# Optimization experiments

Hardware: AMD Instinct MI355X
Metric: run time of the kernel (lower is better)

The kernel has to match this reference:

```python
import jax, jax.numpy as jnp
import numpy as np
import math

B, S, HID = 2, 2048, 1536
H, HD = 12, 128           # num_heads, head_dim
LAT = HID // 8            # latent_dim = 192
ROT = HD // 2             # 64, rotary applied to this half-size subspace


def _make_rotary(seq_len, dim=ROT, base=10000.0):
    # LlamaRotaryEmbedding: inv_freq over dim/2 freqs, emb = cat(sin, cos) -> [1,1,S,dim]
    inv_freq = 1.0 / (base ** (np.arange(0, dim, 2, dtype=np.float32) / dim))
    pos = np.arange(seq_len, dtype=np.float32)
    sincos = np.einsum('i,j->ij', pos, inv_freq)  # [S, dim/2]
    emb = np.concatenate([np.sin(sincos), np.cos(sincos)], axis=-1)  # [S, dim]
    return jnp.asarray(emb)[None, None, :, :]


def setup_inputs() -> dict:
    key = jax.random.key(0)
    ks = jax.random.split(key, 10)
    sd = 0.02
    return {
        'hidden_states': jax.random.normal(ks[0], (B, S, HID), jnp.float32),
        'rotary_emb': _make_rotary(S),
        'W_kv_d':  jax.random.normal(ks[1], (HID, LAT), jnp.float32) * sd,
        'W_q_d':   jax.random.normal(ks[2], (HID, LAT), jnp.float32) * sd,
        'W_k_u':   jax.random.normal(ks[3], (LAT, H * ROT), jnp.float32) * sd,
        'W_q_u':   jax.random.normal(ks[4], (LAT, H * ROT), jnp.float32) * sd,
        'W_v_u':   jax.random.normal(ks[5], (LAT, H * HD), jnp.float32) * sd,
        'W_rope_k': jax.random.normal(ks[6], (HID, HID // 2), jnp.float32) * sd,
        'W_rope_q': jax.random.normal(ks[7], (LAT, HID // 2), jnp.float32) * sd,
        'W_o':     jax.random.normal(ks[8], (HID, HID), jnp.float32) * sd,
    }


def _apply_rope(x, emb):
    # x: [B,S,H,ROT]; emb: [1,1,S,ROT] (cat of sin,cos, each ROT/2)
    half = ROT // 2
    x1, x2 = x[..., :half], x[..., half:]
    sin = emb[..., :half].transpose(0, 2, 1, 3)  # -> [1,S,1,half] to broadcast over heads
    cos = emb[..., half:].transpose(0, 2, 1, 3)
    return jnp.concatenate([x1 * cos - x2 * sin, x1 * sin + x2 * cos], axis=-1)


def reference(hidden_states, rotary_emb, W_kv_d, W_q_d, W_k_u, W_q_u, W_v_u,
              W_rope_k, W_rope_q, W_o):
    b, s, _ = hidden_states.shape
    kv_d = hidden_states @ W_kv_d                       # [B,S,LAT]
    q_d = hidden_states @ W_q_d                         # [B,S,LAT]
    k_c = (kv_d @ W_k_u).reshape(b, s, H, ROT)          # content half of K
    q_c = (q_d @ W_q_u).reshape(b, s, H, ROT)
    v = (kv_d @ W_v_u).reshape(b, s, H, HD)
    k_r = (hidden_states @ W_rope_k).reshape(b, s, H, ROT)
    q_r = (q_d @ W_rope_q).reshape(b, s, H, ROT)
    k_r = _apply_rope(k_r, rotary_emb)
    q_r = _apply_rope(q_r, rotary_emb)
    k = jnp.concatenate([k_c, k_r], axis=-1)            # [B,S,H,HD]
    q = jnp.concatenate([q_c, q_r], axis=-1)

    scores = jnp.einsum('bqhd,bkhd->bhqk', q, k) / math.sqrt(HD)
    causal = jnp.tril(jnp.ones((s, s), dtype=bool))
    scores = jnp.where(causal[None, None], scores, jnp.float32(-1e9))
    probs = jax.nn.softmax(scores, axis=-1)
    attn = jnp.einsum('bhqk,bkhd->bqhd', probs, v).reshape(b, s, HID)
    return attn @ W_o
```

## Files before the change

### kernel.cpp

```cpp
#include <hip/hip_runtime.h>
#include <hip/hip_bf16.h>

#define B_ 2
#define S_ 2048
#define HID_ 1536
#define H_ 12
#define HD_ 128
#define LAT_ 192
#define ROT_ 64
#define M_ (B_*S_)

typedef __hip_bfloat16 bf16;

using short8  = __attribute__((ext_vector_type(8))) short;
using short4v = __attribute__((ext_vector_type(4))) short;
using float4v = __attribute__((ext_vector_type(4))) float;

__device__ __forceinline__ unsigned short f2bf(float f) {
  __hip_bfloat16 h = __float2bfloat16(f);
  unsigned short u; __builtin_memcpy(&u, &h, 2); return u;
}

#define GLDS16(gp, lp) __builtin_amdgcn_global_load_lds( \
    (__attribute__((address_space(1))) void*)(size_t)(gp), \
    (__attribute__((address_space(3))) void*)(lp), 16, 0, 0)

__global__ __launch_bounds__(256)
void fillf_k(float* __restrict__ out, float v, int n)
{
  int i = blockIdx.x*256 + threadIdx.x;
  if (i < n) out[i] = v;
}

__global__ __launch_bounds__(256)
void packT4_k(const float* __restrict__ s0, const float* __restrict__ s1,
              const float* __restrict__ s2, const float* __restrict__ s3,
              bf16* __restrict__ d0, bf16* __restrict__ d1,
              bf16* __restrict__ d2, bf16* __restrict__ d3,
              int Kn, int N0, int N1, int N2, int N3)
{
  const float* W; bf16* Wt; int Nn;
  switch (blockIdx.z) {
    case 0:  W = s0; Wt = d0; Nn = N0; break;
    case 1:  W = s1; Wt = d1; Nn = N1; break;
    case 2:  W = s2; Wt = d2; Nn = N2; break;
    default: W = s3; Wt = d3; Nn = N3; break;
  }
  const int kb = blockIdx.x*32, nb = blockIdx.y*32;
  if (nb >= Nn) return;
  __shared__ float t[32][33];
  const int tx = threadIdx.x & 31, ty = threadIdx.x >> 5;
  #pragma unroll
  for (int i = 0; i < 4; i++)
    t[ty+8*i][tx] = W[(size_t)(kb+ty+8*i)*Nn + nb + tx];
  __syncthreads();
  #pragma unroll
  for (int i = 0; i < 4; i++)
    Wt[(size_t)(nb + ty + 8*i)*Kn + kb + tx] = __float2bfloat16(t[tx][ty+8*i]);
}

template<int CMODE, int BM, int AF32>
__global__ __launch_bounds__(256)
void gemm_mfma(const void* __restrict__ Av, const bf16* __restrict__ Bt,
               void* __restrict__ Cv, void* __restrict__ Cv2,
               const float* __restrict__ emb, int Kn, int lda, int ldb, int ldc)
{
  constexpr int MI  = BM/32;
  constexpr int ITA = BM/32;
  __shared__ bf16 As[(size_t)BM*64];
  __shared__ bf16 Bs[128*64];

  const int tid  = threadIdx.x;
  const int lane = tid & 63;
  const int w    = tid >> 6;
  const int col  = lane & 15, quad = lane >> 4;
  const int wr   = w >> 1, wc = w & 1;
  const size_t m0 = (size_t)blockIdx.y * BM;
  const size_t n0 = (size_t)blockIdx.x * 128;

  const bf16* bg[4];
  #pragma unroll
  for (int it = 0; it < 4; it++) {
    int c = tid + it*256, row = c >> 3, seg = c & 7;
    bg[it] = Bt + (n0 + row)*ldb + (size_t)((seg ^ (row & 7))*8);
  }
  const bf16* ag[ITA];
  const float* asrc = nullptr;
  int arow = 0;
  if constexpr (AF32) {
    arow = tid >> 2;
    const int aseg = tid & 3;
    asrc = (const float*)Av + (m0 + arow)*lda + aseg*16;
  } else {
    #pragma unroll
    for (int it = 0; it < ITA; it++) {
      int c = tid + it*256, row = c >> 3, seg = c & 7;
      ag[it] = (const bf16*)Av + (m0 + row)*lda + (size_t)((seg ^ (row & 7))*8);
    }
  }

  float4v acc[MI][4];
  #pragma unroll
  for (int i=0;i<MI;i++)
    #pragma unroll
    for (int j=0;j<4;j++) acc[i][j] = (float4v){0.f,0.f,0.f,0.f};

  for (int k0 = 0; k0 < Kn; k0 += 64) {
    #pragma unroll
    for (int it = 0; it < 4; it++)
      GLDS16(bg[it] + k0, Bs + (size_t)(tid + it*256)*8);
    if constexpr (AF32) {
      const int aseg = tid & 3;
      float4 f0 = *(const float4*)(asrc + k0);
      float4 f1 = *(const float4*)(asrc + k0 + 4);
      float4 f2 = *(const float4*)(asrc + k0 + 8);
      float4 f3 = *(const float4*)(asrc + k0 + 12);
      short8 h0, h1;
      h0[0]=(short)f2bf(f0.x); h0[1]=(short)f2bf(f0.y);
      h0[2]=(short)f2bf(f0.z); h0[3]=(short)f2bf(f0.w);
      h0[4]=(short)f2bf(f1.x); h0[5]=(short)f2bf(f1.y);
      h0[6]=(short)f2bf(f1.z); h0[7]=(short)f2bf(f1.w);
      h1[0]=(short)f2bf(f2.x); h1[1]=(short)f2bf(f2.y);
      h1[2]=(short)f2bf(f2.z); h1[3]=(short)f2bf(f2.w);
      h1[4]=(short)f2bf(f3.x); h1[5]=(short)f2bf(f3.y);
      h1[6]=(short)f2bf(f3.z); h1[7]=(short)f2bf(f3.w);
      const int sl0 = (aseg*2) ^ (arow & 7), sl1 = (aseg*2+1) ^ (arow & 7);
      *(short8*)&As[arow*64 + sl0*8] = h0;
      *(short8*)&As[arow*64 + sl1*8] = h1;
    } else {
      #pragma unroll
      for (int it = 0; it < ITA; it++)
        GLDS16(ag[it] + k0, As + (size_t)(tid + it*256)*8);
    }
    __syncthreads();

    short8 af[MI][2], bfr[4][2];
    #pragma unroll
    for (int i=0;i<MI;i++) {
      const int ar = wr*(BM/2) + i*16 + col;
      #pragma unroll
      for (int k2=0;k2<2;k2++)
        af[i][k2] = *(const short8*)&As[ar*64 + ((k2*4+quad)^(ar&7))*8];
    }
    #pragma unroll
    for (int j=0;j<4;j++) {
      const int br = wc*64 + j*16 + col;
      #pragma unroll
      for (int k2=0;k2<2;k2++)
        bfr[j][k2] = *(const short8*)&Bs[br*64 + ((k2*4+quad)^(br&7))*8];
    }

    #pragma unroll
    for (int k2=0;k2<2;k2++)
      #pragma unroll
      for (int i=0;i<MI;i++)
        #pragma unroll
        for (int j=0;j<4;j++)
          acc[i][j] = __builtin_amdgcn_mfma_f32_16x16x32_bf16(af[i][k2], bfr[j][k2], acc[i][j], 0,0,0);
    __syncthreads();
  }

  if constexpr (CMODE == 0) {
    #pragma unroll
    for (int i=0;i<MI;i++) {
      const size_t row0 = m0 + wr*(BM/2) + i*16 + quad*4;
      #pragma unroll
      for (int j=0;j<4;j++) {
        const int c = (int)n0 + wc*64 + j*16 + col;
        #pragma unroll
        for (int r=0;r<4;r++)
          ((float*)Cv)[(row0+r)*ldc + c] = acc[i][j][r];
      }
    }
    return;
  }

  constexpr int RBASE = (CMODE == 5) ? 384 : 768;
  if ((int)n0 < RBASE) {
    #pragma unroll
    for (int i=0;i<MI;i++) {
      const size_t row0 = m0 + wr*(BM/2) + i*16 + quad*4;
      #pragma unroll
      for (int j=0;j<4;j++) {
        const int c = (int)n0 + wc*64 + j*16 + col;
        #pragma unroll
        for (int r=0;r<4;r++) {
          const float v = acc[i][j][r];
          if constexpr (CMODE == 5)
            ((bf16*)Cv)[(row0+r)*384 + c] = __float2bfloat16(v);
          else
            ((bf16*)Cv)[(row0+r)*HID_ + (c>>6)*HD_ + (c&63)] = __float2bfloat16(v);
        }
      }
    }
  } else if constexpr (CMODE == 3) {
    #pragma unroll
    for (int i=0;i<MI;i++) {
      const size_t row0 = m0 + wr*(BM/2) + i*16 + quad*4;
      const int bb = (int)(row0 >> 11), s = (int)(row0 & (S_-1));
      #pragma unroll
      for (int j=0;j<4;j++) {
        const int cv = (int)n0 - 768 + wc*64 + j*16 + col;
        const int hh = cv >> 7, d = cv & 127;
        short4v st;
        #pragma unroll
        for (int r=0;r<4;r++) st[r] = (short)f2bf(acc[i][j][r]);
        *(short4v*)((unsigned short*)Cv2 +
            ((size_t)(bb*H_+hh)*HD_ + d)*S_ + s) = st;
      }
    }
  } else {
    const int hh = (((int)n0 - RBASE) >> 6) + wc;
    #pragma unroll
    for (int i=0;i<MI;i++) {
      const size_t row0 = m0 + wr*(BM/2) + i*16 + quad*4;
      #pragma unroll
      for (int j=0;j<2;j++) {
        const int idim = j*16 + col;
        #pragma unroll
        for (int r=0;r<4;r++) {
          const size_t row = row0 + r;
          const int s = (int)(row & (S_-1));
          const float sn = emb[(size_t)s*ROT_ + idim];
          const float cs = emb[(size_t)s*ROT_ + 32 + idim];
          const float x1 = acc[i][j][r], x2 = acc[i][j+2][r];
          bf16* dst = (bf16*)Cv2 + (row*H_ + hh)*HD_ + 64 + idim;
          dst[0]  = __float2bfloat16(x1*cs - x2*sn);
          dst[32] = __float2bfloat16(x1*sn + x2*cs);
        }
      }
    }
  }
}

#define KSTR 136
#define VSTR 72
#define PSTR 72

__global__ __launch_bounds__(256)
void attn_mfma(const bf16* __restrict__ Qf, const bf16* __restrict__ Kf,
               const bf16* __restrict__ Vtg, bf16* __restrict__ at)
{
  const int qt = (S_/64 - 1) - (int)(blockIdx.x / (B_*H_));
  const int bh = blockIdx.x % (B_*H_);
  const int h  = bh % H_, b = bh / H_;
  const int tid  = threadIdx.x;
  const int w    = tid >> 6;
  const int lane = tid & 63;
  const int col  = lane & 15;
  const int quad = lane >> 4;

  __shared__ unsigned short Ks[64*KSTR];
  __shared__ unsigned short Vt[128*VSTR];
  __shared__ unsigned short Ps[4][16*PSTR];

  const int q0  = qt * 64;
  const int q0w = q0 + w*16;

  const unsigned short* Kb = (const unsigned short*)Kf +
      ((size_t)b*S_*H_ + h)*HD_;
  const unsigned short* Vb = (const unsigned short*)Vtg +
      (size_t)(b*H_ + h)*HD_*S_;

  const unsigned short* kgp[4]; unsigned short* kdst[4];
  const unsigned short* vgp[4]; unsigned short* vdst[4];
  #pragma unroll
  for (int it = 0; it < 4; it++) {
    int c = tid + it*256;
    int key = c >> 4, doff = (c & 15)*8;
    kgp[it]  = Kb + (size_t)key*HID_ + doff;
    kdst[it] = &Ks[key*KSTR + doff];
    int d = c >> 3, kg = (c & 7)*8;
    vgp[it]  = Vb + (size_t)d*S_ + kg;
    vdst[it] = &Vt[d*VSTR + kg];
  }

  short8 qf[4];
  {
    const unsigned short* qrow = (const unsigned short*)Qf +
        ((size_t)((size_t)b*S_ + q0w + col)*H_ + h)*HD_;
    #pragma unroll
    for (int kk = 0; kk < 4; kk++)
      qf[kk] = *(const short8*)(qrow + kk*32 + quad*8);
  }

  float4v O[8];
  #pragma unroll
  for (int t=0;t<8;t++) O[t] = (float4v){0.f,0.f,0.f,0.f};
  float m_ln = -1e30f, l_ln = 0.f;

  const float scale2 = 0.08838834764831845f * 1.4426950408889634f;

  short8 kr[4], vr[4];
  #pragma unroll
  for (int it = 0; it < 4; it++) {
    kr[it] = *(const short8*)kgp[it];
    vr[it] = *(const short8*)vgp[it];
  }

  for (int kb = 0; kb <= qt; kb++) {
    const int k0 = kb * 64;
    const bool diag = (kb == qt);

    #pragma unroll
    for (int it = 0; it < 4; it++) *(short8*)kdst[it] = kr[it];
    #pragma unroll
    for (int it = 0; it < 4; it++) *(short8*)vdst[it] = vr[it];
    __syncthreads();

    if (!diag) {
      const size_t kn = (size_t)(k0 + 64);
      #pragma unroll
      for (int it = 0; it < 4; it++) {
        kr[it] = *(const short8*)(kgp[it] + kn*HID_);
        vr[it] = *(const short8*)(vgp[it] + kn);
      }
    }

    float4v Sf[4];
    #pragma unroll
    for (int tc=0;tc<4;tc++) Sf[tc] = (float4v){0.f,0.f,0.f,0.f};
    __builtin_amdgcn_s_setprio(1);
    if (!diag) {
      #pragma unroll
      for (int tc = 0; tc < 4; tc++)
        #pragma unroll
        for (int kk = 0; kk < 4; kk++) {
          short8 kfrag = *(const short8*)&Ks[(16*tc+col)*KSTR + 32*kk + quad*8];
          Sf[tc] = __builtin_amdgcn_mfma_f32_16x16x32_bf16(kfrag, qf[kk], Sf[tc], 0,0,0);
        }
    } else {
      #pragma unroll
      for (int tc = 0; tc < 4; tc++) {
        if (tc <= w) {
          #pragma unroll
          for (int kk = 0; kk < 4; kk++) {
            short8 kfrag = *(const short8*)&Ks[(16*tc+col)*KSTR + 32*kk + quad*8];
            Sf[tc] = __builtin_amdgcn_mfma_f32_16x16x32_bf16(kfrag, qf[kk], Sf[tc], 0,0,0);
          }
        }
      }
    }
    __builtin_amdgcn_s_setprio(0);

    float sv[4][4];
    float pmax = -3.0e38f;
    if (!diag) {
      #pragma unroll
      for (int tc = 0; tc < 4; tc++)
        #pragma unroll
        for (int r = 0; r < 4; r++) {
          float s = Sf[tc][r] * scale2;
          sv[tc][r] = s;
          pmax = fmaxf(pmax, s);
        }
    } else {
      const int qrel = w*16 + col;
      #pragma unroll
      for (int tc = 0; tc < 4; tc++)
        #pragma unroll
        for (int r = 0; r < 4; r++) {
          float s = Sf[tc][r] * scale2;
          if (tc*16 + quad*4 + r > qrel) s = -3.0e38f;
          sv[tc][r] = s;
          pmax = fmaxf(pmax, s);
        }
    }
    pmax = fmaxf(pmax, __shfl_xor(pmax, 16));
    pmax = fmaxf(pmax, __shfl_xor(pmax, 32));

    if (__all(pmax <= m_ln + 11.0f)) {
      float lt = 0.f;
      #pragma unroll
      for (int tc = 0; tc < 4; tc++)
        #pragma unroll
        for (int r = 0; r < 4; r++) {
          sv[tc][r] = exp2f(sv[tc][r] - m_ln);
          lt += sv[tc][r];
        }
      lt += __shfl_xor(lt, 16);
      lt += __shfl_xor(lt, 32);
      l_ln += lt;
    } else {
      const float mnew = fmaxf(m_ln, pmax);
      float lt = 0.f;
      #pragma unroll
      for (int tc = 0; tc < 4; tc++)
        #pragma unroll
        for (int r = 0; r < 4; r++) {
          sv[tc][r] = exp2f(sv[tc][r] - mnew);
          lt += sv[tc][r];
        }
      lt += __shfl_xor(lt, 16);
      lt += __shfl_xor(lt, 32);
      const float al = exp2f(m_ln - mnew);
      l_ln = l_ln * al + lt;
      m_ln = mnew;
      float alr[4];
      #pragma unroll
      for (int r = 0; r < 4; r++) alr[r] = __shfl(al, quad*4 + r);
      #pragma unroll
      for (int t = 0; t < 8; t++)
        #pragma unroll
        for (int r = 0; r < 4; r++) O[t][r] *= alr[r];
    }

    #pragma unroll
    for (int tc = 0; tc < 4; tc++) {
      short4v pw;
      pw[0] = (short)f2bf(sv[tc][0]); pw[1] = (short)f2bf(sv[tc][1]);
      pw[2] = (short)f2bf(sv[tc][2]); pw[3] = (short)f2bf(sv[tc][3]);
      *(short4v*)&Ps[w][col*PSTR + tc*16 + quad*4] = pw;
    }

    __builtin_amdgcn_s_setprio(1);
    if (!diag) {
      #pragma unroll
      for (int ks = 0; ks < 2; ks++) {
        short8 pf = *(const short8*)&Ps[w][col*PSTR + 32*ks + quad*8];
        #pragma unroll
        for (int t = 0; t < 8; t++) {
          short8 vf = *(const short8*)&Vt[(16*t + col)*VSTR + 32*ks + quad*8];
          O[t] = __builtin_amdgcn_mfma_f32_16x16x32_bf16(pf, vf, O[t], 0,0,0);
        }
      }
    } else {
      #pragma unroll
      for (int ks = 0; ks < 2; ks++) {
        if (ks == 0 || w >= 2) {
          short8 pf = *(const short8*)&Ps[w][col*PSTR + 32*ks + quad*8];
          #pragma unroll
          for (int t = 0; t < 8; t++) {
            short8 vf = *(const short8*)&Vt[(16*t + col)*VSTR + 32*ks + quad*8];
            O[t] = __builtin_amdgcn_mfma_f32_16x16x32_bf16(pf, vf, O[t], 0,0,0);
          }
        }
      }
    }
    __builtin_amdgcn_s_setprio(0);
    __syncthreads();
  }

  float lr[4];
  #pragma unroll
  for (int r = 0; r < 4; r++) lr[r] = __shfl(l_ln, quad*4 + r);
  #pragma unroll
  for (int r = 0; r < 4; r++) {
    const float linv = 1.f / lr[r];
    const size_t mq = (size_t)b*S_ + q0w + quad*4 + r;
    bf16* dst = at + mq*HID_ + h*HD_ + col;
    #pragma unroll
    for (int t = 0; t < 8; t++)
      dst[16*t] = __float2bfloat16(O[t][r] * linv);
  }
}

extern "C" void kernel_launch(void* const* d_in, const int* in_sizes, int n_in,
                              void* d_out, int out_size, void* d_ws, size_t ws_size,
                              hipStream_t stream)
{
  float* out = (float*)d_out;

  static const int sz_dict[10] = {6291456,131072,294912,294912,147456,
                                  147456,294912,1179648,147456,2359296};
  int bad = -1;
  if (n_in < 10) bad = 15;
  else {
    for (int i = 0; i < 10; i++)
      if (in_sizes[i] != sz_dict[i]) { bad = i; break; }
  }
  if (bad >= 0) {
    float v = 1.0e6f * (float)(1 + bad);
    if (bad < 10) v += (float)(in_sizes[bad] % 1000000);
    fillf_k<<<(out_size + 255)/256, 256, 0, stream>>>(out, v, out_size);
    return;
  }

  const float* hidden = (const float*)d_in[0];
  const float* emb    = (const float*)d_in[1];
  const float* Wkvd   = (const float*)d_in[2];
  const float* Wqd    = (const float*)d_in[3];
  const float* Wku    = (const float*)d_in[4];
  const float* Wqu    = (const float*)d_in[5];
  const float* Wvu    = (const float*)d_in[6];
  const float* Wrk    = (const float*)d_in[7];
  const float* Wrq    = (const float*)d_in[8];
  const float* Wo     = (const float*)d_in[9];

  char* wp = (char*)d_ws;
  size_t used = 0;
  auto alloc = [&](size_t bytes) -> void* {
    void* p = wp + used;
    used += (bytes + 255) & ~(size_t)255;
    return p;
  };
  bf16*  dout  = (bf16*)alloc((size_t)M_*384*2);
  bf16*  Kf    = (bf16*)alloc((size_t)M_*HID_*2);
  bf16*  Qf    = (bf16*)alloc((size_t)M_*HID_*2);
  bf16*  Vtg   = (bf16*)alloc((size_t)B_*H_*HD_*S_*2);
  bf16*  at    = (bf16*)alloc((size_t)M_*HID_*2);
  bf16*  WdkrT = (bf16*)alloc((size_t)1152*HID_*2);
  bf16*  WkvuT = (bf16*)alloc((size_t)2304*LAT_*2);
  bf16*  WqurT = (bf16*)alloc((size_t)1536*LAT_*2);
  bf16*  WoT   = (bf16*)alloc((size_t)HID_*HID_*2);

  if (used > ws_size) {
    fillf_k<<<(out_size + 255)/256, 256, 0, stream>>>(out, 5.0e7f, out_size);
    return;
  }

  packT4_k<<<dim3(48,48,4), 256, 0, stream>>>(
      Wkvd, Wqd, Wrk, Wo,
      WdkrT, WdkrT + (size_t)192*HID_, WdkrT + (size_t)384*HID_, WoT,
      HID_, LAT_, LAT_, H_*ROT_, HID_);
  packT4_k<<<dim3(6,48,4), 256, 0, stream>>>(
      Wku, Wvu, Wqu, Wrq,
      WkvuT, WkvuT + (size_t)768*LAT_, WqurT, WqurT + (size_t)768*LAT_,
      LAT_, H_*ROT_, HID_, H_*ROT_, H_*ROT_);

  gemm_mfma<5,64,1><<<dim3(9, M_/64),  256, 0, stream>>>(hidden, WdkrT, dout, Kf, emb, HID_, HID_, HID_, 0);
  gemm_mfma<3,64,0><<<dim3(18, M_/64), 256, 0, stream>>>(dout,     WkvuT, Kf, Vtg, emb, LAT_, 384, LAT_, 0);
  gemm_mfma<4,64,0><<<dim3(12, M_/64), 256, 0, stream>>>(dout+192, WqurT, Qf, Qf,  emb, LAT_, 384, LAT_, 0);

  attn_mfma<<<B_*H_*(S_/64), 256, 0, stream>>>(Qf, Kf, Vtg, at);

  gemm_mfma<0,128,0><<<dim3(HID_/128, M_/128), 256, 0, stream>>>(at, WoT, out, nullptr, emb, HID_, HID_, HID_, HID_);
}
```

Measured before the change: 266.5 us.

## Pre-convert hidden to bf16, merge up-projection GEMMs, persistent attention scheduler

Hidden states are converted to bf16 once inside the weight-packing kernel, so the first GEMM loads A through direct global-to-LDS copies and uses 128-row tiles. The two up-projection GEMMs (KV and Q) are merged into a single launch that picks its operands by column range. Attention becomes a persistent kernel of 512 blocks that take tiles from an atomic counter, longest causal tiles first, to balance load. The cost is an extra bf16 copy of the hidden states in memory, a memset, and one atomic per tile.

```diff
diff --git a/kernel.cpp b/kernel.cpp
--- a/kernel.cpp
+++ b/kernel.cpp
@@ -9,6 +9,7 @@
 #define LAT_ 192
 #define ROT_ 64
 #define M_ (B_*S_)
+#define NTILE_ (B_*H_*(S_/64))
 
 typedef __hip_bfloat16 bf16;
 
@@ -33,12 +34,26 @@
 }
 
 __global__ __launch_bounds__(256)
-void packT4_k(const float* __restrict__ s0, const float* __restrict__ s1,
+void packT5_k(const float* __restrict__ s0, const float* __restrict__ s1,
               const float* __restrict__ s2, const float* __restrict__ s3,
               bf16* __restrict__ d0, bf16* __restrict__ d1,
               bf16* __restrict__ d2, bf16* __restrict__ d3,
-              int Kn, int N0, int N1, int N2, int N3)
+              int Kn, int N0, int N1, int N2, int N3,
+              const float* __restrict__ hsrc, bf16* __restrict__ hdst)
 {
+  if (blockIdx.z == 4) {
+    const int nblk = gridDim.x * gridDim.y;
+    const int flatb = blockIdx.y * gridDim.x + blockIdx.x;
+    const float4* in4 = (const float4*)hsrc;
+    for (int i = flatb*256 + threadIdx.x; i < M_*HID_/4; i += nblk*256) {
+      float4 v = in4[i];
+      short4v o;
+      o[0] = (short)f2bf(v.x); o[1] = (short)f2bf(v.y);
+      o[2] = (short)f2bf(v.z); o[3] = (short)f2bf(v.w);
+      *(short4v*)&hdst[i*4] = o;
+    }
+    return;
+  }
   const float* W; bf16* Wt; int Nn;
   switch (blockIdx.z) {
     case 0:  W = s0; Wt = d0; Nn = N0; break;
@@ -59,10 +74,12 @@
     Wt[(size_t)(nb + ty + 8*i)*Kn + kb + tx] = __float2bfloat16(t[tx][ty+8*i]);
 }
 
-template<int CMODE, int BM, int AF32>
+template<int CMODE, int BM>
 __global__ __launch_bounds__(256)
-void gemm_mfma(const void* __restrict__ Av, const bf16* __restrict__ Bt,
+void gemm_mfma(const bf16* __restrict__ Av, const bf16* __restrict__ Btp,
+               const bf16* __restrict__ Av2, const bf16* __restrict__ Bt2,
                void* __restrict__ Cv, void* __restrict__ Cv2,
+               void* __restrict__ Cv3,
                const float* __restrict__ emb, int Kn, int lda, int ldb, int ldc)
 {
   constexpr int MI  = BM/32;
@@ -78,25 +95,24 @@
   const size_t m0 = (size_t)blockIdx.y * BM;
   const size_t n0 = (size_t)blockIdx.x * 128;
 
+  const bf16* Abase = Av;
+  const bf16* Bt    = Btp;
+  size_t nrow0 = n0;
+  if constexpr (CMODE == 6) {
+    if ((int)n0 >= 2304) { Abase = Av2; Bt = Bt2; nrow0 = n0 - 2304; }
+  }
+
   const bf16* bg[4];
   #pragma unroll
   for (int it = 0; it < 4; it++) {
     int c = tid + it*256, row = c >> 3, seg = c & 7;
-    bg[it] = Bt + (n0 + row)*ldb + (size_t)((seg ^ (row & 7))*8);
+    bg[it] = Bt + (nrow0 + row)*ldb + (size_t)((seg ^ (row & 7))*8);
   }
   const bf16* ag[ITA];
-  const float* asrc = nullptr;
-  int arow = 0;
-  if constexpr (AF32) {
-    arow = tid >> 2;
-    const int aseg = tid & 3;
-    asrc = (const float*)Av + (m0 + arow)*lda + aseg*16;
-  } else {
-    #pragma unroll
-    for (int it = 0; it < ITA; it++) {
-      int c = tid + it*256, row = c >> 3, seg = c & 7;
-      ag[it] = (const bf16*)Av + (m0 + row)*lda + (size_t)((seg ^ (row & 7))*8);
-    }
+  #pragma unroll
+  for (int it = 0; it < ITA; it++) {
+    int c = tid + it*256, row = c >> 3, seg = c & 7;
+    ag[it] = Abase + (m0 + row)*lda + (size_t)((seg ^ (row & 7))*8);
   }
 
   float4v acc[MI][4];
@@ -109,29 +125,9 @@
     #pragma unroll
     for (int it = 0; it < 4; it++)
       GLDS16(bg[it] + k0, Bs + (size_t)(tid + it*256)*8);
-    if constexpr (AF32) {
-      const int aseg = tid & 3;
-      float4 f0 = *(const float4*)(asrc + k0);
-      float4 f1 = *(const float4*)(asrc + k0 + 4);
-      float4 f2 = *(const float4*)(asrc + k0 + 8);
-      float4 f3 = *(const float4*)(asrc + k0 + 12);
-      short8 h0, h1;
-      h0[0]=(short)f2bf(f0.x); h0[1]=(short)f2bf(f0.y);
-      h0[2]=(short)f2bf(f0.z); h0[3]=(short)f2bf(f0.w);
-      h0[4]=(short)f2bf(f1.x); h0[5]=(short)f2bf(f1.y);
-      h0[6]=(short)f2bf(f1.z); h0[7]=(short)f2bf(f1.w);
-      h1[0]=(short)f2bf(f2.x); h1[1]=(short)f2bf(f2.y);
-      h1[2]=(short)f2bf(f2.z); h1[3]=(short)f2bf(f2.w);
-      h1[4]=(short)f2bf(f3.x); h1[5]=(short)f2bf(f3.y);
-      h1[6]=(short)f2bf(f3.z); h1[7]=(short)f2bf(f3.w);
-      const int sl0 = (aseg*2) ^ (arow & 7), sl1 = (aseg*2+1) ^ (arow & 7);
-      *(short8*)&As[arow*64 + sl0*8] = h0;
-      *(short8*)&As[arow*64 + sl1*8] = h1;
-    } else {
-      #pragma unroll
-      for (int it = 0; it < ITA; it++)
-        GLDS16(ag[it] + k0, As + (size_t)(tid + it*256)*8);
-    }
+    #pragma unroll
+    for (int it = 0; it < ITA; it++)
+      GLDS16(ag[it] + k0, As + (size_t)(tid + it*256)*8);
     __syncthreads();
 
     short8 af[MI][2], bfr[4][2];
@@ -175,8 +171,45 @@
     return;
   }
 
-  constexpr int RBASE = (CMODE == 5) ? 384 : 768;
-  if ((int)n0 < RBASE) {
+  if constexpr (CMODE == 5) {
+    if ((int)n0 < 384) {
+      #pragma unroll
+      for (int i=0;i<MI;i++) {
+        const size_t row0 = m0 + wr*(BM/2) + i*16 + quad*4;
+        #pragma unroll
+        for (int j=0;j<4;j++) {
+          const int c = (int)n0 + wc*64 + j*16 + col;
+          #pragma unroll
+          for (int r=0;r<4;r++)
+            ((bf16*)Cv)[(row0+r)*384 + c] = __float2bfloat16(acc[i][j][r]);
+        }
+      }
+    } else {
+      const int hh = (((int)n0 - 384) >> 6) + wc;
+      #pragma unroll
+      for (int i=0;i<MI;i++) {
+        const size_t row0 = m0 + wr*(BM/2) + i*16 + quad*4;
+        #pragma unroll
+        for (int j=0;j<2;j++) {
+          const int idim = j*16 + col;
+          #pragma unroll
+          for (int r=0;r<4;r++) {
+            const size_t row = row0 + r;
+            const int s = (int)(row & (S_-1));
+            const float sn = emb[(size_t)s*ROT_ + idim];
+            const float cs = emb[(size_t)s*ROT_ + 32 + idim];
+            const float x1 = acc[i][j][r], x2 = acc[i][j+2][r];
+            bf16* dst = (bf16*)Cv2 + (row*H_ + hh)*HD_ + 64 + idim;
+            dst[0]  = __float2bfloat16(x1*cs - x2*sn);
+            dst[32] = __float2bfloat16(x1*sn + x2*cs);
+          }
+        }
+      }
+    }
+    return;
+  }
+
+  if ((int)n0 < 768) {
     #pragma unroll
     for (int i=0;i<MI;i++) {
       const size_t row0 = m0 + wr*(BM/2) + i*16 + quad*4;
@@ -184,16 +217,11 @@
       for (int j=0;j<4;j++) {
         const int c = (int)n0 + wc*64 + j*16 + col;
         #pragma unroll
-        for (int r=0;r<4;r++) {
-          const float v = acc[i][j][r];
-          if constexpr (CMODE == 5)
-            ((bf16*)Cv)[(row0+r)*384 + c] = __float2bfloat16(v);
-          else
-            ((bf16*)Cv)[(row0+r)*HID_ + (c>>6)*HD_ + (c&63)] = __float2bfloat16(v);
-        }
-      }
-    }
-  } else if constexpr (CMODE == 3) {
+        for (int r=0;r<4;r++)
+          ((bf16*)Cv)[(row0+r)*HID_ + (c>>6)*HD_ + (c&63)] = __float2bfloat16(acc[i][j][r]);
+      }
+    }
+  } else if ((int)n0 < 2304) {
     #pragma unroll
     for (int i=0;i<MI;i++) {
       const size_t row0 = m0 + wr*(BM/2) + i*16 + quad*4;
@@ -209,8 +237,20 @@
             ((size_t)(bb*H_+hh)*HD_ + d)*S_ + s) = st;
       }
     }
+  } else if ((int)n0 < 3072) {
+    #pragma unroll
+    for (int i=0;i<MI;i++) {
+      const size_t row0 = m0 + wr*(BM/2) + i*16 + quad*4;
+      #pragma unroll
+      for (int j=0;j<4;j++) {
+        const int c = (int)n0 - 2304 + wc*64 + j*16 + col;
+        #pragma unroll
+        for (int r=0;r<4;r++)
+          ((bf16*)Cv3)[(row0+r)*HID_ + (c>>6)*HD_ + (c&63)] = __float2bfloat16(acc[i][j][r]);
+      }
+    }
   } else {
-    const int hh = (((int)n0 - RBASE) >> 6) + wc;
+    const int hh = (((int)n0 - 3072) >> 6) + wc;
     #pragma unroll
     for (int i=0;i<MI;i++) {
       const size_t row0 = m0 + wr*(BM/2) + i*16 + quad*4;
@@ -224,7 +264,7 @@
           const float sn = emb[(size_t)s*ROT_ + idim];
           const float cs = emb[(size_t)s*ROT_ + 32 + idim];
           const float x1 = acc[i][j][r], x2 = acc[i][j+2][r];
-          bf16* dst = (bf16*)Cv2 + (row*H_ + hh)*HD_ + 64 + idim;
+          bf16* dst = (bf16*)Cv3 + (row*H_ + hh)*HD_ + 64 + idim;
           dst[0]  = __float2bfloat16(x1*cs - x2*sn);
           dst[32] = __float2bfloat16(x1*sn + x2*cs);
         }
@@ -239,11 +279,9 @@
 
 __global__ __launch_bounds__(256)
 void attn_mfma(const bf16* __restrict__ Qf, const bf16* __restrict__ Kf,
-               const bf16* __restrict__ Vtg, bf16* __restrict__ at)
+               const bf16* __restrict__ Vtg, bf16* __restrict__ at,
+               int* __restrict__ qcnt)
 {
-  const int qt = (S_/64 - 1) - (int)(blockIdx.x / (B_*H_));
-  const int bh = blockIdx.x % (B_*H_);
-  const int h  = bh % H_, b = bh / H_;
   const int tid  = threadIdx.x;
   const int w    = tid >> 6;
   const int lane = tid & 63;
@@ -253,181 +291,180 @@
   __shared__ unsigned short Ks[64*KSTR];
   __shared__ unsigned short Vt[128*VSTR];
   __shared__ unsigned short Ps[4][16*PSTR];
-
-  const int q0  = qt * 64;
-  const int q0w = q0 + w*16;
-
-  const unsigned short* Kb = (const unsigned short*)Kf +
-      ((size_t)b*S_*H_ + h)*HD_;
-  const unsigned short* Vb = (const unsigned short*)Vtg +
-      (size_t)(b*H_ + h)*HD_*S_;
-
-  const unsigned short* kgp[4]; unsigned short* kdst[4];
-  const unsigned short* vgp[4]; unsigned short* vdst[4];
-  #pragma unroll
-  for (int it = 0; it < 4; it++) {
-    int c = tid + it*256;
-    int key = c >> 4, doff = (c & 15)*8;
-    kgp[it]  = Kb + (size_t)key*HID_ + doff;
-    kdst[it] = &Ks[key*KSTR + doff];
-    int d = c >> 3, kg = (c & 7)*8;
-    vgp[it]  = Vb + (size_t)d*S_ + kg;
-    vdst[it] = &Vt[d*VSTR + kg];
-  }
-
-  short8 qf[4];
-  {
-    const unsigned short* qrow = (const unsigned short*)Qf +
-        ((size_t)((size_t)b*S_ + q0w + col)*H_ + h)*HD_;
-    #pragma unroll
-    for (int kk = 0; kk < 4; kk++)
-      qf[kk] = *(const short8*)(qrow + kk*32 + quad*8);
-  }
-
-  float4v O[8];
-  #pragma unroll
-  for (int t=0;t<8;t++) O[t] = (float4v){0.f,0.f,0.f,0.f};
-  float m_ln = -1e30f, l_ln = 0.f;
+  __shared__ int sidx;
 
   const float scale2 = 0.08838834764831845f * 1.4426950408889634f;
 
-  short8 kr[4], vr[4];
-  #pragma unroll
-  for (int it = 0; it < 4; it++) {
-    kr[it] = *(const short8*)kgp[it];
-    vr[it] = *(const short8*)vgp[it];
-  }
-
-  for (int kb = 0; kb <= qt; kb++) {
-    const int k0 = kb * 64;
-    const bool diag = (kb == qt);
-
-    #pragma unroll
-    for (int it = 0; it < 4; it++) *(short8*)kdst[it] = kr[it];
-    #pragma unroll
-    for (int it = 0; it < 4; it++) *(short8*)vdst[it] = vr[it];
+  for (;;) {
+    if (tid == 0) sidx = atomicAdd(qcnt, 1);
     __syncthreads();
-
-    if (!diag) {
-      const size_t kn = (size_t)(k0 + 64);
-      #pragma unroll
-      for (int it = 0; it < 4; it++) {
-        kr[it] = *(const short8*)(kgp[it] + kn*HID_);
-        vr[it] = *(const short8*)(vgp[it] + kn);
-      }
-    }
-
-    float4v Sf[4];
-    #pragma unroll
-    for (int tc=0;tc<4;tc++) Sf[tc] = (float4v){0.f,0.f,0.f,0.f};
-    __builtin_amdgcn_s_setprio(1);
-    if (!diag) {
-      #pragma unroll
-      for (int tc = 0; tc < 4; tc++)
-        #pragma unroll
-        for (int kk = 0; kk < 4; kk++) {
-          short8 kfrag = *(const short8*)&Ks[(16*tc+col)*KSTR + 32*kk + quad*8];
-          Sf[tc] = __builtin_amdgcn_mfma_f32_16x16x32_bf16(kfrag, qf[kk], Sf[tc], 0,0,0);
-        }
-    } else {
-      #pragma unroll
-      for (int tc = 0; tc < 4; tc++) {
-        if (tc <= w) {
+    const int my = sidx;
+    __syncthreads();
+    if (my >= NTILE_) return;
+
+    const int qt = (S_/64 - 1) - my/24;
+    const int bh = my % 24;
+    const int h  = bh % H_, b = bh / H_;
+    const int q0w = qt*64 + w*16;
+
+    const unsigned short* Kb = (const unsigned short*)Kf +
+        ((size_t)b*S_*H_ + h)*HD_;
+    const unsigned short* Vb = (const unsigned short*)Vtg +
+        (size_t)(b*H_ + h)*HD_*S_;
+
+    const unsigned short* kgp[4]; unsigned short* kdst[4];
+    const unsigned short* vgp[4]; unsigned short* vdst[4];
+    #pragma unroll
+    for (int it = 0; it < 4; it++) {
+      int c = tid + it*256;
+      int key = c >> 4, doff = (c & 15)*8;
+      kgp[it]  = Kb + (size_t)key*HID_ + doff;
+      kdst[it] = &Ks[key*KSTR + doff];
+      int d = c >> 3, kg = (c & 7)*8;
+      vgp[it]  = Vb + (size_t)d*S_ + kg;
+      vdst[it] = &Vt[d*VSTR + kg];
+    }
+
+    short8 qf[4];
+    {
+      const unsigned short* qrow = (const unsigned short*)Qf +
+          ((size_t)((size_t)b*S_ + q0w + col)*H_ + h)*HD_;
+      #pragma unroll
+      for (int kk = 0; kk < 4; kk++)
+        qf[kk] = *(const short8*)(qrow + kk*32 + quad*8);
+    }
+
+    float4v O[8];
+    #pragma unroll
+    for (int t=0;t<8;t++) O[t] = (float4v){0.f,0.f,0.f,0.f};
+    float m_ln = -1e30f, l_ln = 0.f;
+
+    short8 kr[4], vr[4];
+    #pragma unroll
+    for (int it = 0; it < 4; it++) {
+      kr[it] = *(const short8*)kgp[it];
+      vr[it] = *(const short8*)vgp[it];
+    }
+
+    for (int kb = 0; kb <= qt; kb++) {
+      const int k0 = kb * 64;
+      const bool diag = (kb == qt);
+
+      #pragma unroll
+      for (int it = 0; it < 4; it++) *(short8*)kdst[it] = kr[it];
+      #pragma unroll
+      for (int it = 0; it < 4; it++) *(short8*)vdst[it] = vr[it];
+      __syncthreads();
+
+      if (!diag) {
+        const size_t kn = (size_t)(k0 + 64);
+        #pragma unroll
+        for (int it = 0; it < 4; it++) {
+          kr[it] = *(const short8*)(kgp[it] + kn*HID_);
+          vr[it] = *(const short8*)(vgp[it] + kn);
+        }
+      }
+
+      float4v Sf[4];
+      #pragma unroll
+      for (int tc=0;tc<4;tc++) Sf[tc] = (float4v){0.f,0.f,0.f,0.f};
+      __builtin_amdgcn_s_setprio(1);
+      if (!diag) {
+        #pragma unroll
+        for (int tc = 0; tc < 4; tc++)
           #pragma unroll
           for (int kk = 0; kk < 4; kk++) {
             short8 kfrag = *(const short8*)&Ks[(16*tc+col)*KSTR + 32*kk + quad*8];
             Sf[tc] = __builtin_amdgcn_mfma_f32_16x16x32_bf16(kfrag, qf[kk], Sf[tc], 0,0,0);
           }
-        }
-      }
-    }
-    __builtin_amdgcn_s_setprio(0);
-
-    float sv[4][4];
-    float pmax = -3.0e38f;
-    if (!diag) {
-      #pragma unroll
-      for (int tc = 0; tc < 4; tc++)
-        #pragma unroll
-        for (int r = 0; r < 4; r++) {
-          float s = Sf[tc][r] * scale2;
-          sv[tc][r] = s;
-          pmax = fmaxf(pmax, s);
-        }
-    } else {
-      const int qrel = w*16 + col;
-      #pragma unroll
-      for (int tc = 0; tc < 4; tc++)
-        #pragma unroll
-        for (int r = 0; r < 4; r++) {
-          float s = Sf[tc][r] * scale2;
-          if (tc*16 + quad*4 + r > qrel) s = -3.0e38f;
-          sv[tc][r] = s;
-          pmax = fmaxf(pmax, s);
-        }
-    }
-    pmax = fmaxf(pmax, __shfl_xor(pmax, 16));
-    pmax = fmaxf(pmax, __shfl_xor(pmax, 32));
-
-    if (__all(pmax <= m_ln + 11.0f)) {
-      float lt = 0.f;
-      #pragma unroll
-      for (int tc = 0; tc < 4; tc++)
-        #pragma unroll
-        for (int r = 0; r < 4; r++) {
-          sv[tc][r] = exp2f(sv[tc][r] - m_ln);
-          lt += sv[tc][r];
-        }
-      lt += __shfl_xor(lt, 16);
-      lt += __shfl_xor(lt, 32);
-      l_ln += lt;
-    } else {
-      const float mnew = fmaxf(m_ln, pmax);
-      float lt = 0.f;
-      #pragma unroll
-      for (int tc = 0; tc < 4; tc++)
-        #pragma unroll
-        for (int r = 0; r < 4; r++) {
-          sv[tc][r] = exp2f(sv[tc][r] - mnew);
-          lt += sv[tc][r];
-        }
-      lt += __shfl_xor(lt, 16);
-      lt += __shfl_xor(lt, 32);
-      const float al = exp2f(m_ln - mnew);
-      l_ln = l_ln * al + lt;
-      m_ln = mnew;
-      float alr[4];
-      #pragma unroll
-      for (int r = 0; r < 4; r++) alr[r] = __shfl(al, quad*4 + r);
-      #pragma unroll
-      for (int t = 0; t < 8; t++)
-        #pragma unroll
-        for (int r = 0; r < 4; r++) O[t][r] *= alr[r];
-    }
-
-    #pragma unroll
-    for (int tc = 0; tc < 4; tc++) {
-      short4v pw;
-      pw[0] = (short)f2bf(sv[tc][0]); pw[1] = (short)f2bf(sv[tc][1]);
-      pw[2] = (short)f2bf(sv[tc][2]); pw[3] = (short)f2bf(sv[tc][3]);
-      *(short4v*)&Ps[w][col*PSTR + tc*16 + quad*4] = pw;
-    }
-
-    __builtin_amdgcn_s_setprio(1);
-    if (!diag) {
-      #pragma unroll
-      for (int ks = 0; ks < 2; ks++) {
-        short8 pf = *(const short8*)&Ps[w][col*PSTR + 32*ks + quad*8];
-        #pragma unroll
-        for (int t = 0; t < 8; t++) {
-          short8 vf = *(const short8*)&Vt[(16*t + col)*VSTR + 32*ks + quad*8];
-          O[t] = __builtin_amdgcn_mfma_f32_16x16x32_bf16(pf, vf, O[t], 0,0,0);
-        }
-      }
-    } else {
-      #pragma unroll
-      for (int ks = 0; ks < 2; ks++) {
-        if (ks == 0 || w >= 2) {
+      } else {
+        #pragma unroll
+        for (int tc = 0; tc < 4; tc++) {
+          if (tc <= w) {
+            #pragma unroll
+            for (int kk = 0; kk < 4; kk++) {
+              short8 kfrag = *(const short8*)&Ks[(16*tc+col)*KSTR + 32*kk + quad*8];
+              Sf[tc] = __builtin_amdgcn_mfma_f32_16x16x32_bf16(kfrag, qf[kk], Sf[tc], 0,0,0);
+            }
+          }
+        }
+      }
+      __builtin_amdgcn_s_setprio(0);
+
+      float sv[4][4];
+      float pmax = -3.0e38f;
+      if (!diag) {
+        #pragma unroll
+        for (int tc = 0; tc < 4; tc++)
+          #pragma unroll
+          for (int r = 0; r < 4; r++) {
+            float s = Sf[tc][r] * scale2;
+            sv[tc][r] = s;
+            pmax = fmaxf(pmax, s);
+          }
+      } else {
+        const int qrel = w*16 + col;
+        #pragma unroll
+        for (int tc = 0; tc < 4; tc++)
+          #pragma unroll
+          for (int r = 0; r < 4; r++) {
+            float s = Sf[tc][r] * scale2;
+            if (tc*16 + quad*4 + r > qrel) s = -3.0e38f;
+            sv[tc][r] = s;
+            pmax = fmaxf(pmax, s);
+          }
+      }
+      pmax = fmaxf(pmax, __shfl_xor(pmax, 16));
+      pmax = fmaxf(pmax, __shfl_xor(pmax, 32));
+
+      if (__all(pmax <= m_ln + 11.0f)) {
+        float lt = 0.f;
+        #pragma unroll
+        for (int tc = 0; tc < 4; tc++)
+          #pragma unroll
+          for (int r = 0; r < 4; r++) {
+            sv[tc][r] = exp2f(sv[tc][r] - m_ln);
+            lt += sv[tc][r];
+          }
+        lt += __shfl_xor(lt, 16);
+        lt += __shfl_xor(lt, 32);
+        l_ln += lt;
+      } else {
+        const float mnew = fmaxf(m_ln, pmax);
+        float lt = 0.f;
+        #pragma unroll
+        for (int tc = 0; tc < 4; tc++)
+          #pragma unroll
+          for (int r = 0; r < 4; r++) {
+            sv[tc][r] = exp2f(sv[tc][r] - mnew);
+            lt += sv[tc][r];
+          }
+        lt += __shfl_xor(lt, 16);
+        lt += __shfl_xor(lt, 32);
+        const float al = exp2f(m_ln - mnew);
+        l_ln = l_ln * al + lt;
+        m_ln = mnew;
+        float alr[4];
+        #pragma unroll
+        for (int r = 0; r < 4; r++) alr[r] = __shfl(al, quad*4 + r);
+        #pragma unroll
+        for (int t = 0; t < 8; t++)
+          #pragma unroll
+          for (int r = 0; r < 4; r++) O[t][r] *= alr[r];
+      }
+
+      #pragma unroll
+      for (int tc = 0; tc < 4; tc++) {
+        short4v pw;
+        pw[0] = (short)f2bf(sv[tc][0]); pw[1] = (short)f2bf(sv[tc][1]);
+        pw[2] = (short)f2bf(sv[tc][2]); pw[3] = (short)f2bf(sv[tc][3]);
+        *(short4v*)&Ps[w][col*PSTR + tc*16 + quad*4] = pw;
+      }
+
+      __builtin_amdgcn_s_setprio(1);
+      if (!diag) {
+        #pragma unroll
+        for (int ks = 0; ks < 2; ks++) {
           short8 pf = *(const short8*)&Ps[w][col*PSTR + 32*ks + quad*8];
           #pragma unroll
           for (int t = 0; t < 8; t++) {
@@ -435,23 +472,35 @@
             O[t] = __builtin_amdgcn_mfma_f32_16x16x32_bf16(pf, vf, O[t], 0,0,0);
           }
         }
-      }
-    }
-    __builtin_amdgcn_s_setprio(0);
-    __syncthreads();
-  }
-
-  float lr[4];
-  #pragma unroll
-  for (int r = 0; r < 4; r++) lr[r] = __shfl(l_ln, quad*4 + r);
-  #pragma unroll
-  for (int r = 0; r < 4; r++) {
-    const float linv = 1.f / lr[r];
-    const size_t mq = (size_t)b*S_ + q0w + quad*4 + r;
-    bf16* dst = at + mq*HID_ + h*HD_ + col;
-    #pragma unroll
-    for (int t = 0; t < 8; t++)
-      dst[16*t] = __float2bfloat16(O[t][r] * linv);
+      } else {
+        #pragma unroll
+        for (int ks = 0; ks < 2; ks++) {
+          if (ks == 0 || w >= 2) {
+            short8 pf = *(const short8*)&Ps[w][col*PSTR + 32*ks + quad*8];
+            #pragma unroll
+            for (int t = 0; t < 8; t++) {
+              short8 vf = *(const short8*)&Vt[(16*t + col)*VSTR + 32*ks + quad*8];
+              O[t] = __builtin_amdgcn_mfma_f32_16x16x32_bf16(pf, vf, O[t], 0,0,0);
+            }
+          }
+        }
+      }
+      __builtin_amdgcn_s_setprio(0);
+      __syncthreads();
+    }
+
+    float lr[4];
+    #pragma unroll
+    for (int r = 0; r < 4; r++) lr[r] = __shfl(l_ln, quad*4 + r);
+    #pragma unroll
+    for (int r = 0; r < 4; r++) {
+      const float linv = 1.f / lr[r];
+      const size_t mq = (size_t)b*S_ + q0w + quad*4 + r;
+      bf16* dst = at + mq*HID_ + h*HD_ + col;
+      #pragma unroll
+      for (int t = 0; t < 8; t++)
+        dst[16*t] = __float2bfloat16(O[t][r] * linv);
+    }
   }
 }
 
@@ -494,6 +543,7 @@
     used += (bytes + 255) & ~(size_t)255;
     return p;
   };
+  bf16*  hb    = (bf16*)alloc((size_t)M_*HID_*2);
   bf16*  dout  = (bf16*)alloc((size_t)M_*384*2);
   bf16*  Kf    = (bf16*)alloc((size_t)M_*HID_*2);
   bf16*  Qf    = (bf16*)alloc((size_t)M_*HID_*2);
@@ -503,26 +553,33 @@
   bf16*  WkvuT = (bf16*)alloc((size_t)2304*LAT_*2);
   bf16*  WqurT = (bf16*)alloc((size_t)1536*LAT_*2);
   bf16*  WoT   = (bf16*)alloc((size_t)HID_*HID_*2);
+  int*   qcnt  = (int*)alloc(256);
 
   if (used > ws_size) {
     fillf_k<<<(out_size + 255)/256, 256, 0, stream>>>(out, 5.0e7f, out_size);
     return;
   }
 
-  packT4_k<<<dim3(48,48,4), 256, 0, stream>>>(
+  hipMemsetAsync(qcnt, 0, sizeof(int), stream);
+
+  packT5_k<<<dim3(48,48,5), 256, 0, stream>>>(
       Wkvd, Wqd, Wrk, Wo,
       WdkrT, WdkrT + (size_t)192*HID_, WdkrT + (size_t)384*HID_, WoT,
-      HID_, LAT_, LAT_, H_*ROT_, HID_);
-  packT4_k<<<dim3(6,48,4), 256, 0, stream>>>(
+      HID_, LAT_, LAT_, H_*ROT_, HID_,
+      hidden, hb);
+  packT5_k<<<dim3(6,48,4), 256, 0, stream>>>(
       Wku, Wvu, Wqu, Wrq,
       WkvuT, WkvuT + (size_t)768*LAT_, WqurT, WqurT + (size_t)768*LAT_,
-      LAT_, H_*ROT_, HID_, H_*ROT_, H_*ROT_);
-
-  gemm_mfma<5,64,1><<<dim3(9, M_/64),  256, 0, stream>>>(hidden, WdkrT, dout, Kf, emb, HID_, HID_, HID_, 0);
-  gemm_mfma<3,64,0><<<dim3(18, M_/64), 256, 0, stream>>>(dout,     WkvuT, Kf, Vtg, emb, LAT_, 384, LAT_, 0);
-  gemm_mfma<4,64,0><<<dim3(12, M_/64), 256, 0, stream>>>(dout+192, WqurT, Qf, Qf,  emb, LAT_, 384, LAT_, 0);
-
-  attn_mfma<<<B_*H_*(S_/64), 256, 0, stream>>>(Qf, Kf, Vtg, at);
-
-  gemm_mfma<0,128,0><<<dim3(HID_/128, M_/128), 256, 0, stream>>>(at, WoT, out, nullptr, emb, HID_, HID_, HID_, HID_);
+      LAT_, H_*ROT_, HID_, H_*ROT_, H_*ROT_,
+      nullptr, nullptr);
+
+  gemm_mfma<5,128><<<dim3(9, M_/128), 256, 0, stream>>>(
+      hb, WdkrT, nullptr, nullptr, dout, Kf, nullptr, emb, HID_, HID_, HID_, 0);
+  gemm_mfma<6,128><<<dim3(30, M_/128), 256, 0, stream>>>(
+      dout, WkvuT, dout + 192, WqurT, Kf, Vtg, Qf, emb, LAT_, 384, LAT_, 0);
+
+  attn_mfma<<<512, 256, 0, stream>>>(Qf, Kf, Vtg, at, qcnt);
+
+  gemm_mfma<0,128><<<dim3(HID_/128, M_/128), 256, 0, stream>>>(
+      at, WoT, nullptr, nullptr, out, nullptr, nullptr, emb, HID_, HID_, HID_, HID_);
 }
```

Result: no change. 261.9 us (-1.7%).
